# Optimization experiments

Hardware: AMD Instinct MI355X
Metric: run time of the kernel (lower is better)

The kernel has to match this reference:

```python
import jax, jax.numpy as jnp
import numpy as np

HIDDEN = 128
NUM_BLOCKS = 8
BLOCK = HIDDEN // NUM_BLOCKS  # 16
HSF = 1                       # hidden_size_factor
LAMBDA = 0.01                 # sparsity_threshold (softshrink)
SCALE = 0.02


def softshrink(v, lam):
    return jnp.sign(v) * jnp.maximum(jnp.abs(v) - lam, 0.0)


def setup_inputs() -> dict:
    key = jax.random.key(0)
    k0, k1, k2, k3, k4 = jax.random.split(key, 5)
    x = jax.random.normal(k0, (4, HIDDEN, 256, 256), dtype=jnp.float32)
    w1 = SCALE * jax.random.normal(k1, (2, NUM_BLOCKS, BLOCK, BLOCK * HSF), dtype=jnp.float32)
    b1 = SCALE * jax.random.normal(k2, (2, NUM_BLOCKS, BLOCK * HSF), dtype=jnp.float32)
    w2 = SCALE * jax.random.normal(k3, (2, NUM_BLOCKS, BLOCK * HSF, BLOCK), dtype=jnp.float32)
    b2 = SCALE * jax.random.normal(k4, (2, NUM_BLOCKS, BLOCK), dtype=jnp.float32)
    return {"x": x, "w1": w1, "b1": b1, "w2": w2, "b2": b2}


def reference(x, w1, b1, w2, b2):
    bias = x
    B, C, H, W = x.shape
    xf = jnp.fft.rfft2(x.astype(jnp.float32), axes=(2, 3), norm='ortho')  # [B,C,H,Wf] complex
    Wf = xf.shape[3]
    xb = xf.reshape(B, NUM_BLOCKS, BLOCK, H, Wf)
    xr, xi = xb.real, xb.imag

    mm = lambda a, w: jnp.einsum('bkihw,kio->bkohw', a, w)
    o1r = jax.nn.relu(mm(xr, w1[0]) - mm(xi, w1[1]) + b1[0][None, :, :, None, None])
    o1i = jax.nn.relu(mm(xi, w1[0]) + mm(xr, w1[1]) + b1[1][None, :, :, None, None])
    o2r = mm(o1r, w2[0]) - mm(o1i, w2[1]) + b2[0][None, :, :, None, None]
    o2i = mm(o1i, w2[0]) + mm(o1r, w2[1]) + b2[1][None, :, :, None, None]

    sr = softshrink(o2r, LAMBDA)
    si = softshrink(o2i, LAMBDA)
    xc = (sr + 1j * si).reshape(B, C, H, Wf) * xf
    out = jnp.fft.irfft2(xc, s=(H, W), axes=(2, 3), norm='ortho').astype(x.dtype)
    return out + bias
```

## Files before the change

kernel.cpp:

```cpp
#include <hip/hip_runtime.h>
#include <math.h>

#define Bn 4
#define Cn 128
#define Hn 256
#define Wn 256
#define WFn 129
#define NBn 8
#define BLn 16
#define LAMv 0.01f
#define LSTR 272

#define C1c 0.9238795325112867f
#define S1c 0.3826834323650898f
#define RTc 0.7071067811865476f

__device__ constexpr int rev4(int j) {
  return ((j & 1) << 3) | ((j & 2) << 1) | ((j & 4) >> 1) | ((j & 8) >> 3);
}

__device__ __forceinline__ float2 pkfma(float2 a, float2 b, float2 c) {
  return make_float2(fmaf(a.x, b.x, c.x), fmaf(a.y, b.y, c.y));
}

template <int SIGN>
__device__ __forceinline__ void fft16(float* xr, float* xi) {
  const float g = (SIGN > 0) ? 1.0f : -1.0f;
  {
    const float WC[8] = {1.f, C1c, RTc, S1c, 0.f, -S1c, -RTc, -C1c};
    const float WS[8] = {0.f, -S1c, -RTc, -C1c, -1.f, -C1c, -RTc, -S1c};
#pragma unroll
    for (int j = 0; j < 8; j++) {
      float ur = xr[j], ui = xi[j], vr = xr[j + 8], vi = xi[j + 8];
      float dr = ur - vr, di = ui - vi;
      xr[j] = ur + vr; xi[j] = ui + vi;
      float wc = WC[j], ws = g * WS[j];
      xr[j + 8] = dr * wc - di * ws;
      xi[j + 8] = dr * ws + di * wc;
    }
  }
  {
    const float WC[4] = {1.f, RTc, 0.f, -RTc};
    const float WS[4] = {0.f, -RTc, -1.f, -RTc};
#pragma unroll
    for (int b = 0; b < 16; b += 8)
#pragma unroll
      for (int j = 0; j < 4; j++) {
        float ur = xr[b + j], ui = xi[b + j];
        float vr = xr[b + j + 4], vi = xi[b + j + 4];
        float dr = ur - vr, di = ui - vi;
        xr[b + j] = ur + vr; xi[b + j] = ui + vi;
        float wc = WC[j], ws = g * WS[j];
        xr[b + j + 4] = dr * wc - di * ws;
        xi[b + j + 4] = dr * ws + di * wc;
      }
  }
  {
#pragma unroll
    for (int b = 0; b < 16; b += 4) {
      {
        float ur = xr[b], ui = xi[b], vr = xr[b + 2], vi = xi[b + 2];
        xr[b] = ur + vr; xi[b] = ui + vi;
        xr[b + 2] = ur - vr; xi[b + 2] = ui - vi;
      }
      {
        float ur = xr[b + 1], ui = xi[b + 1], vr = xr[b + 3], vi = xi[b + 3];
        float dr = ur - vr, di = ui - vi;
        xr[b + 1] = ur + vr; xi[b + 1] = ui + vi;
        xr[b + 3] = g * di;
        xi[b + 3] = -g * dr;
      }
    }
  }
  {
#pragma unroll
    for (int b = 0; b < 16; b += 2) {
      float ur = xr[b], ui = xi[b], vr = xr[b + 1], vi = xi[b + 1];
      xr[b] = ur + vr; xi[b] = ui + vi;
      xr[b + 1] = ur - vr; xi[b + 1] = ui - vi;
    }
  }
}

template <int SIGN>
__device__ __forceinline__ void fft256_4step(float* vr, float* vi,
                                             float* re, float* im, int s) {
  fft16<SIGN>(vr, vi);
  const float fs = (float)s;
#pragma unroll
  for (int j = 1; j < 16; j++) {
    const int k2 = rev4(j);
    float sn, cs;
    sincospif(fs * ((float)k2 / 128.0f), &sn, &cs);
    float ws = (SIGN > 0) ? -sn : sn;
    float r = vr[j] * cs - vi[j] * ws;
    vi[j] = vr[j] * ws + vi[j] * cs;
    vr[j] = r;
  }
  __syncthreads();
#pragma unroll
  for (int j = 0; j < 16; j++) {
    const int k2 = rev4(j);
    const int p = k2 * 16 + (s ^ k2);
    re[p] = vr[j]; im[p] = vi[j];
  }
  __syncthreads();
#pragma unroll
  for (int n1 = 0; n1 < 16; n1++) {
    const int p = s * 16 + (n1 ^ s);
    vr[n1] = re[p]; vi[n1] = im[p];
  }
  __syncthreads();
  fft16<SIGN>(vr, vi);
}

__global__ __launch_bounds__(256) void k_rowfft(const float* __restrict__ x,
                                                float2* __restrict__ S) {
  int blk = blockIdx.x;
  int bc = blk >> 3;
  int h0 = (blk & 7) << 5;
  __shared__ __align__(16) float zr[16][LSTR], zi[16][LSTR];
  int t = threadIdx.x;
  const float4* xrow =
      (const float4*)(x + (size_t)bc * (Hn * Wn) + (size_t)h0 * Wn);
  const float sc = 1.0f / 256.0f;
#pragma unroll
  for (int j = 0; j < 8; j++) {
    int f4 = t + j * 256;
    float4 v = xrow[f4];
    int r = f4 >> 6;
    int i = (f4 << 2) & 255;
    float* dst = (r & 1) ? &zi[r >> 1][i] : &zr[r >> 1][i];
    *(float4*)dst = make_float4(v.x * sc, v.y * sc, v.z * sc, v.w * sc);
  }
  __syncthreads();
  int p = t >> 4, s = t & 15;
  float vr[16], vi[16];
#pragma unroll
  for (int m = 0; m < 16; m++) {
    vr[m] = zr[p][s + 16 * m];
    vi[m] = zi[p][s + 16 * m];
  }
  fft256_4step<1>(vr, vi, &zr[p][0], &zi[p][0], s);
#pragma unroll
  for (int j = 0; j < 16; j++) {
    int h = 16 * rev4(j) + s;
    zr[p][h] = vr[j]; zi[p][h] = vi[j];
  }
  __syncthreads();
  for (int f = t; f < WFn * 32; f += 256) {
    int wf = f >> 5, rr = f & 31;
    int pp = rr >> 1;
    int nk = (256 - wf) & 255;
    float zkr = zr[pp][wf], zki = zi[pp][wf];
    float znr = zr[pp][nk], zni = zi[pp][nk];
    float re_, im_;
    if ((rr & 1) == 0) { re_ = 0.5f * (zkr + znr); im_ = 0.5f * (zki - zni); }
    else               { re_ = 0.5f * (zki + zni); im_ = 0.5f * (znr - zkr); }
    S[((size_t)bc * WFn + wf) * Hn + (h0 + rr)] = make_float2(re_, im_);
  }
}

__global__ __launch_bounds__(256) void k_spectral(float2* __restrict__ S,
                                                  const float* __restrict__ w1,
                                                  const float* __restrict__ b1,
                                                  const float* __restrict__ w2,
                                                  const float* __restrict__ b2) {
  int blk = blockIdx.x;
  int wcol = blk % WFn;
  int bk = blk / WFn;
  int k = bk & 7;
  int b = bk >> 3;
  __shared__ __align__(16) float ar[16][LSTR], ai[16][LSTR];
  __shared__ __align__(16) float w1r[256], w1i[256], w2r[256], w2i[256];
  __shared__ float b1r[16], b1i[16], b2r[16], b2i[16];
  int t = threadIdx.x;
  w1r[t] = w1[k * 256 + t];        w1i[t] = w1[(8 + k) * 256 + t];
  w2r[t] = w2[k * 256 + t];        w2i[t] = w2[(8 + k) * 256 + t];
  if (t < 16) {
    b1r[t] = b1[k * 16 + t];       b1i[t] = b1[(8 + k) * 16 + t];
    b2r[t] = b2[k * 16 + t];       b2i[t] = b2[(8 + k) * 16 + t];
  }
  int c = t >> 4, s = t & 15;
  float2* col = S + ((size_t)(b * Cn + k * BLn + c) * WFn + wcol) * Hn;
  float vr[16], vi[16];
#pragma unroll
  for (int m = 0; m < 16; m++) {
    float2 z = col[s + 16 * m];
    vr[m] = z.x; vi[m] = z.y;
  }
  fft256_4step<1>(vr, vi, &ar[c][0], &ai[c][0], s);
#pragma unroll
  for (int j = 0; j < 16; j++) {
    int h = 16 * rev4(j) + s;
    ar[c][h] = vr[j]; ai[c][h] = vi[j];
  }
  __syncthreads();

  {
    const int h = t;
    const float4* W1R = (const float4*)w1r;
    const float4* W1I = (const float4*)w1i;
    const float4* W2R = (const float4*)w2r;
    const float4* W2I = (const float4*)w2i;
    float2 o1p[8], o1q[8];
#pragma unroll
    for (int q = 0; q < 8; q++) {
      o1p[q] = make_float2(b1r[2 * q], b1r[2 * q + 1]);
      o1q[q] = make_float2(b1i[2 * q], b1i[2 * q + 1]);
    }
#pragma unroll
    for (int i = 0; i < 16; i++) {
      float xr_ = ar[i][h], xi_ = ai[i][h];
      float2 xr2 = make_float2(xr_, xr_);
      float2 xi2 = make_float2(xi_, xi_);
      float2 xn2 = make_float2(-xi_, -xi_);
#pragma unroll
      for (int oq = 0; oq < 4; oq++) {
        float4 wr = W1R[i * 4 + oq];
        float4 wi = W1I[i * 4 + oq];
        float2 wr0 = make_float2(wr.x, wr.y), wr1 = make_float2(wr.z, wr.w);
        float2 wi0 = make_float2(wi.x, wi.y), wi1 = make_float2(wi.z, wi.w);
        o1p[2 * oq + 0] = pkfma(xr2, wr0, pkfma(xn2, wi0, o1p[2 * oq + 0]));
        o1p[2 * oq + 1] = pkfma(xr2, wr1, pkfma(xn2, wi1, o1p[2 * oq + 1]));
        o1q[2 * oq + 0] = pkfma(xi2, wr0, pkfma(xr2, wi0, o1q[2 * oq + 0]));
        o1q[2 * oq + 1] = pkfma(xi2, wr1, pkfma(xr2, wi1, o1q[2 * oq + 1]));
      }
    }
#pragma unroll
    for (int q = 0; q < 8; q++) {
      o1p[q] = make_float2(fmaxf(o1p[q].x, 0.f), fmaxf(o1p[q].y, 0.f));
      o1q[q] = make_float2(fmaxf(o1q[q].x, 0.f), fmaxf(o1q[q].y, 0.f));
    }
    float2 o2p[8], o2q[8];
#pragma unroll
    for (int q = 0; q < 8; q++) {
      o2p[q] = make_float2(b2r[2 * q], b2r[2 * q + 1]);
      o2q[q] = make_float2(b2i[2 * q], b2i[2 * q + 1]);
    }
#pragma unroll
    for (int i = 0; i < 16; i++) {
      float pr = (i & 1) ? o1p[i >> 1].y : o1p[i >> 1].x;
      float pi_ = (i & 1) ? o1q[i >> 1].y : o1q[i >> 1].x;
      float2 pr2 = make_float2(pr, pr);
      float2 pi2 = make_float2(pi_, pi_);
      float2 pn2 = make_float2(-pi_, -pi_);
#pragma unroll
      for (int oq = 0; oq < 4; oq++) {
        float4 wr = W2R[i * 4 + oq];
        float4 wi = W2I[i * 4 + oq];
        float2 wr0 = make_float2(wr.x, wr.y), wr1 = make_float2(wr.z, wr.w);
        float2 wi0 = make_float2(wi.x, wi.y), wi1 = make_float2(wi.z, wi.w);
        o2p[2 * oq + 0] = pkfma(pr2, wr0, pkfma(pn2, wi0, o2p[2 * oq + 0]));
        o2p[2 * oq + 1] = pkfma(pr2, wr1, pkfma(pn2, wi1, o2p[2 * oq + 1]));
        o2q[2 * oq + 0] = pkfma(pi2, wr0, pkfma(pr2, wi0, o2q[2 * oq + 0]));
        o2q[2 * oq + 1] = pkfma(pi2, wr1, pkfma(pr2, wi1, o2q[2 * oq + 1]));
      }
    }
#pragma unroll
    for (int o = 0; o < 16; o++) {
      float vr_ = (o & 1) ? o2p[o >> 1].y : o2p[o >> 1].x;
      float vi_ = (o & 1) ? o2q[o >> 1].y : o2q[o >> 1].x;
      float sr = copysignf(fmaxf(fabsf(vr_) - LAMv, 0.0f), vr_);
      float si = copysignf(fmaxf(fabsf(vi_) - LAMv, 0.0f), vi_);
      float fr = ar[o][h], fi = ai[o][h];
      ar[o][h] = sr * fr - si * fi;
      ai[o][h] = sr * fi + si * fr;
    }
  }
  __syncthreads();
#pragma unroll
  for (int m = 0; m < 16; m++) {
    vr[m] = ar[c][s + 16 * m];
    vi[m] = ai[c][s + 16 * m];
  }
  fft256_4step<-1>(vr, vi, &ar[c][0], &ai[c][0], s);
#pragma unroll
  for (int j = 0; j < 16; j++) {
    int h = 16 * rev4(j) + s;
    col[h] = make_float2(vr[j], vi[j]);
  }
}

__global__ __launch_bounds__(256) void k_invrow(const float2* __restrict__ S,
                                                const float* __restrict__ x,
                                                float* __restrict__ out) {
  int blk = blockIdx.x;
  int bc = blk >> 4;
  int h0 = (blk & 15) << 4;
  __shared__ __align__(16) float ar[16][LSTR], ai[16][LSTR];
  int t = threadIdx.x;
  for (int f = t; f < WFn * 16; f += 256) {
    int wf = f >> 4, rr = f & 15;
    float2 v = S[((size_t)bc * WFn + wf) * Hn + (h0 + rr)];
    ar[rr][wf] = v.x; ai[rr][wf] = v.y;
  }
  __syncthreads();
  for (int m = t; m < 127 * 16; m += 256) {
    int wf = 129 + (m >> 4), rr = m & 15;
    ar[rr][wf] = ar[rr][256 - wf];
    ai[rr][wf] = -ai[rr][256 - wf];
  }
  __syncthreads();
  int r = t >> 4, s = t & 15;
  float vr[16], vi[16];
#pragma unroll
  for (int m = 0; m < 16; m++) {
    vr[m] = ar[r][s + 16 * m];
    vi[m] = ai[r][s + 16 * m];
  }
  fft256_4step<-1>(vr, vi, &ar[r][0], &ai[r][0], s);
#pragma unroll
  for (int j = 0; j < 16; j++) {
    ar[r][16 * rev4(j) + s] = vr[j];
  }
  __syncthreads();
  const float sc = 1.0f / 256.0f;
  size_t base = (size_t)bc * (Hn * Wn) + (size_t)h0 * Wn;
  const float4* x4 = (const float4*)(x + base);
  float4* o4 = (float4*)(out + base);
#pragma unroll
  for (int j = 0; j < 4; j++) {
    int f4 = t + j * 256;
    int rr = f4 >> 6, i = (f4 << 2) & 255;
    float4 v = *(const float4*)&ar[rr][i];
    float4 xv = x4[f4];
    o4[f4] = make_float4(fmaf(v.x, sc, xv.x), fmaf(v.y, sc, xv.y),
                         fmaf(v.z, sc, xv.z), fmaf(v.w, sc, xv.w));
  }
}

extern "C" void kernel_launch(void* const* d_in, const int* in_sizes, int n_in,
                              void* d_out, int out_size, void* d_ws,
                              size_t ws_size, hipStream_t stream) {
  const float* x  = (const float*)d_in[0];
  const float* w1 = (const float*)d_in[1];
  const float* b1 = (const float*)d_in[2];
  const float* w2 = (const float*)d_in[3];
  const float* b2 = (const float*)d_in[4];
  float* out = (float*)d_out;
  float2* S = (float2*)d_ws;

  k_rowfft<<<Bn * Cn * (Hn / 32), 256, 0, stream>>>(x, S);
  k_spectral<<<Bn * NBn * WFn, 256, 0, stream>>>(S, w1, b1, w2, b2);
  k_invrow<<<Bn * Cn * (Hn / 16), 256, 0, stream>>>(S, x, out);
}
```

Baseline: 446.9 us.

## Precompute FFT twiddles in LDS and pack two real rows per inverse FFT

Replaces the per-thread sincospif twiddle calls in the 256-point four-step FFT with a 256-entry twiddle table in shared memory, computed once per block. It also restructures the inverse row kernel to process two real rows per complex FFT, packing the two Hermitian spectra as Z = A + iB. This halves the number of inverse row FFTs and doubles the rows per block. The cost is extra LDS traffic for twiddle reads and one more barrier, and the packing logic has to be exactly right for correctness.

```diff
diff --git a/kernel.cpp b/kernel.cpp
--- a/kernel.cpp
+++ b/kernel.cpp
@@ -23,6 +23,13 @@
   return make_float2(fmaf(a.x, b.x, c.x), fmaf(a.y, b.y, c.y));
 }
 
+__device__ __forceinline__ void init_twt(float2* twt, int t) {
+  int s = t >> 4, k2 = t & 15;
+  float sn, cs;
+  sincospif((float)(s * k2) / 128.0f, &sn, &cs);
+  twt[t] = make_float2(cs, -sn);
+}
+
 template <int SIGN>
 __device__ __forceinline__ void fft16(float* xr, float* xi) {
   const float g = (SIGN > 0) ? 1.0f : -1.0f;
@@ -84,17 +91,17 @@
 
 template <int SIGN>
 __device__ __forceinline__ void fft256_4step(float* vr, float* vi,
-                                             float* re, float* im, int s) {
+                                             float* re, float* im, int s,
+                                             const float2* twt) {
   fft16<SIGN>(vr, vi);
-  const float fs = (float)s;
 #pragma unroll
   for (int j = 1; j < 16; j++) {
     const int k2 = rev4(j);
-    float sn, cs;
-    sincospif(fs * ((float)k2 / 128.0f), &sn, &cs);
-    float ws = (SIGN > 0) ? -sn : sn;
-    float r = vr[j] * cs - vi[j] * ws;
-    vi[j] = vr[j] * ws + vi[j] * cs;
+    float2 w = twt[s * 16 + k2];
+    float wc = w.x;
+    float ws = (SIGN > 0) ? w.y : -w.y;
+    float r = vr[j] * wc - vi[j] * ws;
+    vi[j] = vr[j] * ws + vi[j] * wc;
     vr[j] = r;
   }
   __syncthreads();
@@ -120,7 +127,9 @@
   int bc = blk >> 3;
   int h0 = (blk & 7) << 5;
   __shared__ __align__(16) float zr[16][LSTR], zi[16][LSTR];
+  __shared__ __align__(16) float2 twt[256];
   int t = threadIdx.x;
+  init_twt(&twt[0], t);
   const float4* xrow =
       (const float4*)(x + (size_t)bc * (Hn * Wn) + (size_t)h0 * Wn);
   const float sc = 1.0f / 256.0f;
@@ -141,7 +150,7 @@
     vr[m] = zr[p][s + 16 * m];
     vi[m] = zi[p][s + 16 * m];
   }
-  fft256_4step<1>(vr, vi, &zr[p][0], &zi[p][0], s);
+  fft256_4step<1>(vr, vi, &zr[p][0], &zi[p][0], s, &twt[0]);
 #pragma unroll
   for (int j = 0; j < 16; j++) {
     int h = 16 * rev4(j) + s;
@@ -172,15 +181,18 @@
   int k = bk & 7;
   int b = bk >> 3;
   __shared__ __align__(16) float ar[16][LSTR], ai[16][LSTR];
+  __shared__ __align__(16) float2 twt[256];
   __shared__ __align__(16) float w1r[256], w1i[256], w2r[256], w2i[256];
   __shared__ float b1r[16], b1i[16], b2r[16], b2i[16];
   int t = threadIdx.x;
+  init_twt(&twt[0], t);
   w1r[t] = w1[k * 256 + t];        w1i[t] = w1[(8 + k) * 256 + t];
   w2r[t] = w2[k * 256 + t];        w2i[t] = w2[(8 + k) * 256 + t];
   if (t < 16) {
     b1r[t] = b1[k * 16 + t];       b1i[t] = b1[(8 + k) * 16 + t];
     b2r[t] = b2[k * 16 + t];       b2i[t] = b2[(8 + k) * 16 + t];
   }
+  __syncthreads();
   int c = t >> 4, s = t & 15;
   float2* col = S + ((size_t)(b * Cn + k * BLn + c) * WFn + wcol) * Hn;
   float vr[16], vi[16];
@@ -189,7 +201,7 @@
     float2 z = col[s + 16 * m];
     vr[m] = z.x; vi[m] = z.y;
   }
-  fft256_4step<1>(vr, vi, &ar[c][0], &ai[c][0], s);
+  fft256_4step<1>(vr, vi, &ar[c][0], &ai[c][0], s, &twt[0]);
 #pragma unroll
   for (int j = 0; j < 16; j++) {
     int h = 16 * rev4(j) + s;
@@ -274,7 +286,7 @@
     vr[m] = ar[c][s + 16 * m];
     vi[m] = ai[c][s + 16 * m];
   }
-  fft256_4step<-1>(vr, vi, &ar[c][0], &ai[c][0], s);
+  fft256_4step<-1>(vr, vi, &ar[c][0], &ai[c][0], s, &twt[0]);
 #pragma unroll
   for (int j = 0; j < 16; j++) {
     int h = 16 * rev4(j) + s;
@@ -286,33 +298,36 @@
                                                 const float* __restrict__ x,
                                                 float* __restrict__ out) {
   int blk = blockIdx.x;
-  int bc = blk >> 4;
-  int h0 = (blk & 15) << 4;
-  __shared__ __align__(16) float ar[16][LSTR], ai[16][LSTR];
+  int bc = blk >> 3;
+  int h0 = (blk & 7) << 5;
+  __shared__ __align__(16) float zr[16][LSTR], zi[16][LSTR];
+  __shared__ __align__(16) float2 twt[256];
   int t = threadIdx.x;
+  init_twt(&twt[0], t);
+  const float4* S4 = (const float4*)S;
   for (int f = t; f < WFn * 16; f += 256) {
-    int wf = f >> 4, rr = f & 15;
-    float2 v = S[((size_t)bc * WFn + wf) * Hn + (h0 + rr)];
-    ar[rr][wf] = v.x; ai[rr][wf] = v.y;
-  }
-  __syncthreads();
-  for (int m = t; m < 127 * 16; m += 256) {
-    int wf = 129 + (m >> 4), rr = m & 15;
-    ar[rr][wf] = ar[rr][256 - wf];
-    ai[rr][wf] = -ai[rr][256 - wf];
-  }
-  __syncthreads();
-  int r = t >> 4, s = t & 15;
+    int wf = f >> 4, p = f & 15;
+    float4 v = S4[((size_t)bc * WFn + wf) * (Hn / 2) + (h0 >> 1) + p];
+    zr[p][wf] = v.x - v.w;
+    zi[p][wf] = v.y + v.z;
+    if (wf >= 1 && wf <= 127) {
+      zr[p][256 - wf] = v.x + v.w;
+      zi[p][256 - wf] = v.z - v.y;
+    }
+  }
+  __syncthreads();
+  int p = t >> 4, s = t & 15;
   float vr[16], vi[16];
 #pragma unroll
   for (int m = 0; m < 16; m++) {
-    vr[m] = ar[r][s + 16 * m];
-    vi[m] = ai[r][s + 16 * m];
-  }
-  fft256_4step<-1>(vr, vi, &ar[r][0], &ai[r][0], s);
-#pragma unroll
-  for (int j = 0; j < 16; j++) {
-    ar[r][16 * rev4(j) + s] = vr[j];
+    vr[m] = zr[p][s + 16 * m];
+    vi[m] = zi[p][s + 16 * m];
+  }
+  fft256_4step<-1>(vr, vi, &zr[p][0], &zi[p][0], s, &twt[0]);
+#pragma unroll
+  for (int j = 0; j < 16; j++) {
+    int w = 16 * rev4(j) + s;
+    zr[p][w] = vr[j]; zi[p][w] = vi[j];
   }
   __syncthreads();
   const float sc = 1.0f / 256.0f;
@@ -320,10 +335,12 @@
   const float4* x4 = (const float4*)(x + base);
   float4* o4 = (float4*)(out + base);
 #pragma unroll
-  for (int j = 0; j < 4; j++) {
+  for (int j = 0; j < 8; j++) {
     int f4 = t + j * 256;
-    int rr = f4 >> 6, i = (f4 << 2) & 255;
-    float4 v = *(const float4*)&ar[rr][i];
+    int rr = f4 >> 6;
+    int i = (f4 << 2) & 255;
+    const float* src = (rr & 1) ? &zi[rr >> 1][i] : &zr[rr >> 1][i];
+    float4 v = *(const float4*)src;
     float4 xv = x4[f4];
     o4[f4] = make_float4(fmaf(v.x, sc, xv.x), fmaf(v.y, sc, xv.y),
                          fmaf(v.z, sc, xv.z), fmaf(v.w, sc, xv.w));
@@ -343,5 +360,5 @@
 
   k_rowfft<<<Bn * Cn * (Hn / 32), 256, 0, stream>>>(x, S);
   k_spectral<<<Bn * NBn * WFn, 256, 0, stream>>>(S, w1, b1, w2, b2);
-  k_invrow<<<Bn * Cn * (Hn / 16), 256, 0, stream>>>(S, x, out);
-}
+  k_invrow<<<Bn * Cn * (Hn / 32), 256, 0, stream>>>(S, x, out);
+}
```

New measurement: 458.5 us. +2.6%, slower.
